# Kernel tuning notes

Measured on AMD Instinct MI355X. Metric: run time of the kernel, lower is better.

Reference implementation:

```python
import jax, jax.numpy as jnp
import numpy as np

# Static problem sizes (must match setup_inputs)
B = 4                 # batch (scenes)
N_POINTS = 524288     # total points across batch (data_dict['feats'].shape[0])
NUM_PROPOSAL = 256    # fixed slots per scene (self.num_proposal)
FEAT_DIM = 16         # hard-coded in torch.zeros(..., 16)


def setup_inputs() -> dict:
    key = jax.random.key(0)
    k1, k2, k3 = jax.random.split(key, 3)
    P = 256            # total proposals across batch
    PPB = P // B       # proposals per scene = 64 (< NUM_PROPOSAL -> no topk branch)
    PTS_PER_BATCH = N_POINTS // B
    PPP = 4096         # points per proposal
    M = P * PPP
    K_INST = 32        # max GT instances per scene (ious second dim)

    rng = np.random.RandomState(0)
    pid = np.repeat(np.arange(P), PPP)                     # (M,) proposal id, sorted
    bat = pid // PPB                                       # scene of each entry
    ptid = rng.randint(0, PTS_PER_BATCH, size=M) + bat * PTS_PER_BATCH
    proposals_idx = np.stack([pid, ptid], axis=1).astype(np.int64)   # (M, 2)
    proposals_offset = (np.arange(P + 1) * PPP).astype(np.int64)     # (P+1,)
    batch_offsets = (np.arange(B + 1) * PTS_PER_BATCH).astype(np.int64)  # (B+1,)

    return {
        "scores": jax.random.normal(k1, (P, 1), dtype=jnp.float32),
        "score_feats": jax.random.normal(k2, (P, FEAT_DIM), dtype=jnp.float32),
        "ious": jax.random.uniform(k3, (P, K_INST), dtype=jnp.float32),
        "proposals_idx": jnp.asarray(proposals_idx),
        "proposals_offset": jnp.asarray(proposals_offset),
        "batch_offsets": jnp.asarray(batch_offsets),
    }


def reference(scores, score_feats, ious, proposals_idx, proposals_offset, batch_offsets):
    P = score_feats.shape[0]

    # scores_pred = sigmoid(scores.view(-1))
    scores_pred = jax.nn.sigmoid(scores.reshape(-1))                      # (P,)

    # proposals_pred[pid, ptid] = 1  -- big irregular scatter, (P, N) int32
    proposals_pred = jnp.zeros((P, N_POINTS), dtype=jnp.int32)
    proposals_pred = proposals_pred.at[proposals_idx[:, 0], proposals_idx[:, 1]].set(1)

    # batch index of each proposal from the first point in the proposal
    # (equivalent to the python boundary-search loop over batch_offsets)
    first_pt = proposals_idx[proposals_offset[:-1], 1]                    # (P,)
    b_idx = jnp.searchsorted(batch_offsets, first_pt, side="right") - 1   # (P,) in [0,B)

    # slot of each proposal within its scene (rank of appearance, loop order)
    onehot = jax.nn.one_hot(b_idx, B, dtype=jnp.int32)                    # (P, B)
    slot = jnp.cumsum(onehot, axis=0)[jnp.arange(P), b_idx] - 1           # (P,)

    # pack into fixed-size per-scene tensors (topk overflow branch not taken:
    # per-scene count <= NUM_PROPOSAL by construction, matching common path)
    batch = jnp.zeros((B, NUM_PROPOSAL, FEAT_DIM), dtype=score_feats.dtype)
    batch = batch.at[b_idx, slot].set(score_feats)

    proposal_mask = jnp.zeros((B, NUM_PROPOSAL), dtype=jnp.float32)
    proposal_mask = proposal_mask.at[b_idx, slot].set(1.0)

    K_INST = ious.shape[1]
    proposal_ious = jnp.zeros((B, NUM_PROPOSAL, K_INST), dtype=ious.dtype)
    proposal_ious = proposal_ious.at[b_idx, slot].set(ious)

    return batch, proposal_mask, scores_pred, proposal_ious, proposals_pred
```

## Files before the change

### kernel.cpp

```cpp
#include <hip/hip_runtime.h>


#define N_POINTS_C 524288
#define NUM_PROPOSAL_C 256
#define FEAT_DIM_C 16

__global__ void proposal_small_kernel(const float* __restrict__ scores,
                                      const float* __restrict__ feats,
                                      const float* __restrict__ ious,
                                      const int* __restrict__ pidx,
                                      const int* __restrict__ poff,
                                      const int* __restrict__ boff,
                                      int P, int nB, int K,
                                      float* __restrict__ out_batch,
                                      float* __restrict__ out_mask,
                                      float* __restrict__ out_spred,
                                      float* __restrict__ out_ious) {
    __shared__ int sb[NUM_PROPOSAL_C];
    const int p = threadIdx.x;
    int b = 0;
    if (p < P) {
        const int fp = pidx[2 * poff[p] + 1];
        b = nB - 1;
        for (int j = 0; j < nB; ++j) {
            if (fp < boff[j + 1]) { b = j; break; }
        }
        sb[p] = b;
    }
    __syncthreads();
    if (p < P) {
        int slot = 0;
        for (int q = 0; q < p; ++q) slot += (sb[q] == b) ? 1 : 0;

        out_mask[b * NUM_PROPOSAL_C + slot] = 1.0f;
        out_spred[p] = 1.0f / (1.0f + expf(-scores[p]));

        const int dst_bs = b * NUM_PROPOSAL_C + slot;
        #pragma unroll
        for (int j = 0; j < FEAT_DIM_C; ++j)
            out_batch[dst_bs * FEAT_DIM_C + j] = feats[p * FEAT_DIM_C + j];
        for (int j = 0; j < K; ++j)
            out_ious[dst_bs * K + j] = ious[p * K + j];
    }
}

__global__ void scatter_ones_kernel(const int2* __restrict__ pidx,
                                    float* __restrict__ out_pp,
                                    int M) {
    const int i = blockIdx.x * blockDim.x + threadIdx.x;
    if (i < M) {
        const int2 e = pidx[i];
        out_pp[(size_t)e.x * N_POINTS_C + e.y] = 1.0f;
    }
}

extern "C" void kernel_launch(void* const* d_in, const int* in_sizes, int n_in,
                              void* d_out, int out_size, void* d_ws, size_t ws_size,
                              hipStream_t stream) {
    const float* scores = (const float*)d_in[0];
    const float* feats  = (const float*)d_in[1];
    const float* ious   = (const float*)d_in[2];
    const int*   pidx   = (const int*)d_in[3];
    const int*   poff   = (const int*)d_in[4];
    const int*   boff   = (const int*)d_in[5];

    const int P  = in_sizes[0];
    const int K  = in_sizes[2] / P;
    const int M  = in_sizes[3] / 2;
    const int nB = in_sizes[5] - 1;

    float* out = (float*)d_out;
    float* out_batch = out;
    float* out_mask  = out_batch + (size_t)nB * NUM_PROPOSAL_C * FEAT_DIM_C;
    float* out_spred = out_mask  + (size_t)nB * NUM_PROPOSAL_C;
    float* out_ious  = out_spred + P;
    float* out_pp    = out_ious  + (size_t)nB * NUM_PROPOSAL_C * K;

    hipMemsetAsync(d_out, 0, (size_t)out_size * sizeof(float), stream);

    proposal_small_kernel<<<1, 256, 0, stream>>>(scores, feats, ious, pidx,
                                                 poff, boff, P, nB, K,
                                                 out_batch, out_mask,
                                                 out_spred, out_ious);

    const int threads = 256;
    const int blocks  = (M + threads - 1) / threads;
    scatter_ones_kernel<<<blocks, threads, 0, stream>>>((const int2*)pidx,
                                                        out_pp, M);
}
```

Measured before the change: 584.9 us.

## Build per-proposal LDS bitmap and write dense mask once instead of memset+scatter

```diff
diff --git a/kernel.cpp b/kernel.cpp
--- a/kernel.cpp
+++ b/kernel.cpp
@@ -4,6 +4,8 @@
 #define N_POINTS_C 524288
 #define NUM_PROPOSAL_C 256
 #define FEAT_DIM_C 16
+#define SPLIT 2
+#define HALF_WORDS (N_POINTS_C / 32 / SPLIT)
 
 __global__ void proposal_small_kernel(const float* __restrict__ scores,
                                       const float* __restrict__ feats,
@@ -18,6 +20,16 @@
                                       float* __restrict__ out_ious) {
     __shared__ int sb[NUM_PROPOSAL_C];
     const int p = threadIdx.x;
+
+    {
+        const int nbatch = nB * NUM_PROPOSAL_C * FEAT_DIM_C;
+        for (int i = p; i < nbatch; i += blockDim.x) out_batch[i] = 0.0f;
+        const int nmask = nB * NUM_PROPOSAL_C;
+        for (int i = p; i < nmask; i += blockDim.x) out_mask[i] = 0.0f;
+        const int nious = nB * NUM_PROPOSAL_C * K;
+        for (int i = p; i < nious; i += blockDim.x) out_ious[i] = 0.0f;
+    }
+
     int b = 0;
     if (p < P) {
         const int fp = pidx[2 * poff[p] + 1];
@@ -44,13 +56,44 @@
     }
 }
 
-__global__ void scatter_ones_kernel(const int2* __restrict__ pidx,
-                                    float* __restrict__ out_pp,
-                                    int M) {
-    const int i = blockIdx.x * blockDim.x + threadIdx.x;
-    if (i < M) {
-        const int2 e = pidx[i];
-        out_pp[(size_t)e.x * N_POINTS_C + e.y] = 1.0f;
+__global__ __launch_bounds__(1024, 2)
+void proposals_pred_kernel(const int* __restrict__ pidx,
+                           const int* __restrict__ poff,
+                           float* __restrict__ out_pp) {
+    __shared__ unsigned bm[HALF_WORDS];
+    const int p    = blockIdx.x / SPLIT;
+    const int part = blockIdx.x % SPLIT;
+    const int tid  = threadIdx.x;
+    const int lo   = part * (N_POINTS_C / SPLIT);
+    const int hi   = lo + (N_POINTS_C / SPLIT);
+
+    #pragma unroll
+    for (int w = tid; w < HALF_WORDS; w += 1024) bm[w] = 0u;
+    __syncthreads();
+
+    const int s = poff[p];
+    const int e = poff[p + 1];
+    for (int i = s + tid; i < e; i += 1024) {
+        const int pt = pidx[2 * i + 1];
+        if (pt >= lo && pt < hi) {
+            const int rel = pt - lo;
+            atomicOr(&bm[rel >> 5], 1u << (rel & 31));
+        }
+    }
+    __syncthreads();
+
+    float4* dst = (float4*)(out_pp + (size_t)p * N_POINTS_C + lo);
+    const int nvec = (N_POINTS_C / SPLIT) / 4;
+    #pragma unroll 4
+    for (int v = tid; v < nvec; v += 1024) {
+        const unsigned w = bm[v >> 3];
+        const int sh = (v & 7) * 4;
+        float4 o;
+        o.x = ((w >> (sh + 0)) & 1u) ? 1.0f : 0.0f;
+        o.y = ((w >> (sh + 1)) & 1u) ? 1.0f : 0.0f;
+        o.z = ((w >> (sh + 2)) & 1u) ? 1.0f : 0.0f;
+        o.w = ((w >> (sh + 3)) & 1u) ? 1.0f : 0.0f;
+        dst[v] = o;
     }
 }
 
@@ -66,7 +109,6 @@
 
     const int P  = in_sizes[0];
     const int K  = in_sizes[2] / P;
-    const int M  = in_sizes[3] / 2;
     const int nB = in_sizes[5] - 1;
 
     float* out = (float*)d_out;
@@ -76,15 +118,10 @@
     float* out_ious  = out_spred + P;
     float* out_pp    = out_ious  + (size_t)nB * NUM_PROPOSAL_C * K;
 
-    hipMemsetAsync(d_out, 0, (size_t)out_size * sizeof(float), stream);
-
     proposal_small_kernel<<<1, 256, 0, stream>>>(scores, feats, ious, pidx,
                                                  poff, boff, P, nB, K,
                                                  out_batch, out_mask,
                                                  out_spred, out_ious);
 
-    const int threads = 256;
-    const int blocks  = (M + threads - 1) / threads;
-    scatter_ones_kernel<<<blocks, threads, 0, stream>>>((const int2*)pidx,
-                                                        out_pp, M);
+    proposals_pred_kernel<<<P * SPLIT, 1024, 0, stream>>>(pidx, poff, out_pp);
 }
```

New measurement: 551.3 us. -5.7%, faster.
